# Kernel optimization log

Hardware: AMD Instinct MI355X
Metric: run time of the kernel (lower is better)

## Reference

```python
import jax, jax.numpy as jnp
import numpy as np

NEG = -10000.0

def setup_inputs() -> dict:
    key = jax.random.key(0)
    ks = jax.random.split(key, 8)
    B, S, D = 16, 1024, 768
    scale = 1.0 / np.sqrt(D)
    return {
        "q": jax.random.normal(ks[0], (B, S, D), jnp.float32),
        "k": jax.random.normal(ks[1], (B, S, D), jnp.float32),
        "v": jax.random.normal(ks[2], (B, S, D), jnp.float32),
        "Wq": jax.random.normal(ks[3], (D, D), jnp.float32) * scale,
        "bq": jnp.zeros((D,), jnp.float32),
        "Wk": jax.random.normal(ks[4], (D, D), jnp.float32) * scale,
        "bk": jnp.zeros((D,), jnp.float32),
        "Wv": jax.random.normal(ks[5], (D, D), jnp.float32) * scale,
        "bv": jnp.zeros((D,), jnp.float32),
        "temperature": jnp.float32(1.0),
    }

def reference(q, k, v, Wq, bq, Wk, bk, Wv, bv, temperature):
    # Linear projections (torch Linear: x @ W.T + b; here W stored as [out,in])
    Q = jnp.einsum("bsd,ed->bse", q, Wq) + bq  # [B,S,Dq]
    K = jnp.einsum("bsd,ed->bse", k, Wk) + bk  # [B,S,Dk]
    V = jnp.einsum("bsd,ed->bse", v, Wv) + bv  # [B,S,Dv]
    scores = jnp.einsum("bqe,bke->bqk", Q, K) / temperature  # [B,S,S]
    S = scores.shape[-1]
    diag = jnp.eye(S, dtype=bool)  # diagonal self-exclusion mask
    scores = jnp.where(diag[None, :, :], NEG, scores)
    attn = jax.nn.softmax(scores, axis=-1)
    return jnp.einsum("bqk,bke->bqe", attn, V)
```

## Files before the change

kernel.cpp:

```cpp
#include <hip/hip_runtime.h>
#include <math.h>


typedef _Float16 f16x8 __attribute__((ext_vector_type(8)));
typedef _Float16 f16x4 __attribute__((ext_vector_type(4)));
typedef __attribute__((ext_vector_type(4))) float f32x4;

template<typename T>
__device__ __forceinline__ void async_copy16(T* lds, const T* g) {
    __builtin_amdgcn_global_load_lds(
        (const __attribute__((address_space(1))) unsigned int*)g,
        (__attribute__((address_space(3))) unsigned int*)lds, 16, 0, 0);
}

__device__ __forceinline__ void barrier_mem() {
    asm volatile("s_barrier" ::: "memory");
}

template<int EPI, int BIAS>
__global__ __launch_bounds__(512, 2)
void mfma_gemm256(const _Float16* __restrict__ A, const _Float16* __restrict__ B,
                  const float* __restrict__ bias, void* __restrict__ C0,
                  int K, int lda, int ldb, int ldc,
                  long long sA, long long sB, long long sC)
{
    __shared__ _Float16 smem[65536];

    const int tid = threadIdx.x;

    const int gx = gridDim.x, gy = gridDim.y;
    const int nwg = gx * gy * gridDim.z;
    const int p = blockIdx.x + gx * (blockIdx.y + gy * blockIdx.z);
    const int cpx = nwg >> 3;
    const int l = (nwg & 7) ? p : (p & 7) * cpx + (p >> 3);
    const int bx = l % gx;
    const int by = (l / gx) % gy;
    const long long bz = l / (gx * gy);
    const int m0 = by * 256, n0 = bx * 256;

    const _Float16* A0 = A + bz * sA;
    const _Float16* B0 = B + bz * sB;

    const int lane = tid & 63;
    const int wid  = tid >> 6;
    const int wm   = wid >> 2;
    const int wn   = wid & 3;
    const int fr   = lane & 15;
    const int fs   = lane >> 4;

    const int nt = K / 64;
    const int iters = nt / 2;

    auto stage_unit = [&](int dbuf, int isB, int unit, int tile) {
        if (tile >= nt) return;
        const int kt = tile * 64;
        const int lr = tid >> 3, s = tid & 7;
        const int grow = isB ? (unit * 64 + lr)
                             : (((lr >> 5) << 7) + unit * 32 + (lr & 31));
        const int gslot = s ^ (grow & 7);
        _Float16* dst = smem + dbuf * 32768 + isB * 16384 + grow * 64 + s * 8;
        const _Float16* src = (isB ? B0 : A0)
            + (size_t)((isB ? n0 : m0) + grow) * (size_t)(isB ? ldb : lda)
            + kt + gslot * 8;
        async_copy16(dst, src);
    };

    f32x4 acc[8][4] = {};
    f16x8 bf[4][2];

#define PHASE(BUF, Q, READB, STAGES, VMW) do {                                 \
    const _Float16* Ab = smem + (BUF) * 32768;                                 \
    const _Float16* Bb = Ab + 16384;                                           \
    f16x8 a0k0, a0k1, a1k0, a1k1;                                              \
    { const int r = wm * 128 + ((Q) * 2 + 0) * 16 + fr;                        \
      a0k0 = *(const f16x8*)&Ab[r * 64 + ((fs       ^ (r & 7)) * 8)];          \
      a0k1 = *(const f16x8*)&Ab[r * 64 + (((4 + fs) ^ (r & 7)) * 8)]; }        \
    { const int r = wm * 128 + ((Q) * 2 + 1) * 16 + fr;                        \
      a1k0 = *(const f16x8*)&Ab[r * 64 + ((fs       ^ (r & 7)) * 8)];          \
      a1k1 = *(const f16x8*)&Ab[r * 64 + (((4 + fs) ^ (r & 7)) * 8)]; }        \
    if (READB) {                                                               \
      _Pragma("unroll") for (int ni = 0; ni < 4; ++ni) {                       \
        const int r = wn * 64 + ni * 16 + fr;                                  \
        bf[ni][0] = *(const f16x8*)&Bb[r * 64 + ((fs       ^ (r & 7)) * 8)];   \
        bf[ni][1] = *(const f16x8*)&Bb[r * 64 + (((4 + fs) ^ (r & 7)) * 8)]; } \
    }                                                                          \
    STAGES;                                                                    \
    barrier_mem();                                                             \
    __builtin_amdgcn_s_setprio(1);                                             \
    _Pragma("unroll") for (int ni = 0; ni < 4; ++ni) {                         \
      acc[(Q)*2+0][ni] = __builtin_amdgcn_mfma_f32_16x16x32_f16(a0k0, bf[ni][0], acc[(Q)*2+0][ni], 0, 0, 0); \
      acc[(Q)*2+0][ni] = __builtin_amdgcn_mfma_f32_16x16x32_f16(a0k1, bf[ni][1], acc[(Q)*2+0][ni], 0, 0, 0); \
      acc[(Q)*2+1][ni] = __builtin_amdgcn_mfma_f32_16x16x32_f16(a1k0, bf[ni][0], acc[(Q)*2+1][ni], 0, 0, 0); \
      acc[(Q)*2+1][ni] = __builtin_amdgcn_mfma_f32_16x16x32_f16(a1k1, bf[ni][1], acc[(Q)*2+1][ni], 0, 0, 0); \
    }                                                                          \
    __builtin_amdgcn_s_setprio(0);                                             \
    VMW;                                                                       \
    barrier_mem();                                                             \
} while (0)

    stage_unit(0, 0, 0, 0); stage_unit(0, 0, 1, 0);
    stage_unit(0, 0, 2, 0); stage_unit(0, 0, 3, 0);
    stage_unit(0, 1, 0, 0); stage_unit(0, 1, 1, 0);
    stage_unit(0, 1, 2, 0); stage_unit(0, 1, 3, 0);
    stage_unit(1, 1, 0, 1); stage_unit(1, 1, 1, 1);
    stage_unit(1, 1, 2, 1); stage_unit(1, 1, 3, 1);
    stage_unit(1, 0, 0, 1); stage_unit(1, 0, 1, 1);
    asm volatile("s_waitcnt vmcnt(6)" ::: "memory");
    barrier_mem();

    for (int i = 0; i < iters; ++i) {
        const int T1 = 2 * i + 1, T2 = 2 * i + 2, T3 = 2 * i + 3;
        const bool last = (i + 1 == iters);
        PHASE(0, 0, 1, stage_unit(1, 0, 2, T1); stage_unit(1, 0, 3, T1), );
        PHASE(0, 1, 0, stage_unit(0, 1, 0, T2); stage_unit(0, 1, 1, T2), );
        PHASE(0, 2, 0, stage_unit(0, 1, 2, T2); stage_unit(0, 1, 3, T2), );
        PHASE(0, 3, 0, stage_unit(0, 0, 0, T2); stage_unit(0, 0, 1, T2),
              if (last) { asm volatile("s_waitcnt vmcnt(0)" ::: "memory"); }
              else      { asm volatile("s_waitcnt vmcnt(6)" ::: "memory"); });
        PHASE(1, 0, 1, stage_unit(0, 0, 2, T2); stage_unit(0, 0, 3, T2), );
        PHASE(1, 1, 0, stage_unit(1, 1, 0, T3); stage_unit(1, 1, 1, T3), );
        PHASE(1, 2, 0, stage_unit(1, 1, 2, T3); stage_unit(1, 1, 3, T3), );
        PHASE(1, 3, 0, stage_unit(1, 0, 0, T3); stage_unit(1, 0, 1, T3),
              asm volatile("s_waitcnt vmcnt(6)" ::: "memory"));
    }
#undef PHASE

    #pragma unroll
    for (int mi = 0; mi < 8; ++mi) {
        #pragma unroll
        for (int ni = 0; ni < 4; ++ni) {
            const int col = n0 + wn * 64 + ni * 16 + fr;
            #pragma unroll
            for (int r = 0; r < 4; ++r) {
                const int row = m0 + wm * 128 + mi * 16 + fs * 4 + r;
                float vv = acc[mi][ni][r];
                if (BIAS == 1) vv += bias[col];
                if (BIAS == 2) vv += bias[row];
                const size_t idx = (size_t)bz * sC + (size_t)row * ldc + col;
                if (EPI == 0) ((float*)C0)[idx] = vv;
                else          ((_Float16*)C0)[idx] = (_Float16)vv;
            }
        }
    }
}

template<int EPI, int BIAS>
__global__ __launch_bounds__(256, 2)
void mfma_gemm(const _Float16* __restrict__ A, const _Float16* __restrict__ B,
               const float* __restrict__ bias,
               void* __restrict__ C0,
               int K, int lda, int ldb, int ldc,
               long long sA, long long sB, long long sC)
{
    __shared__ _Float16 sAh[128 * 32];
    __shared__ _Float16 sBh[128 * 32];

    const int tid = threadIdx.x;
    const int gx = gridDim.x, gy = gridDim.y;
    const int nwg = gx * gy * gridDim.z;
    const int p = blockIdx.x + gx * (blockIdx.y + gy * blockIdx.z);
    const int cpx = nwg >> 3;
    const int l = (nwg & 7) ? p : (p & 7) * cpx + (p >> 3);
    const int bx = l % gx;
    const int by = (l / gx) % gy;
    const long long bz = l / (gx * gy);

    const int m0 = by * 128;
    const int n0 = bx * 128;

    const _Float16* A0 = A + bz * sA;
    const _Float16* B0 = B + bz * sB;

    const int lrow  = tid >> 2;
    const int lslot = tid & 3;

    const int lane = tid & 63;
    const int wv   = tid >> 6;
    const int wm   = wv >> 1, wn = wv & 1;
    const int fr   = lane & 15;
    const int fs   = lane >> 4;
    const int sw   = fs ^ (fr & 3);
    const int abase = (wm * 64 + fr) * 32 + sw * 8;
    const int bbase = (wn * 64 + fr) * 32 + sw * 8;

    f32x4 acc[4][4] = {};

    for (int kt = 0; kt < K; kt += 32) {
        #pragma unroll
        for (int it = 0; it < 2; ++it) {
            const int row = lrow + it * 64;
            const int gsl = (lslot ^ (row & 3)) << 3;
            const size_t loff = (size_t)tid * 8 + (size_t)it * 2048;
            async_copy16(&sAh[loff], A0 + (size_t)(m0 + row) * lda + kt + gsl);
            async_copy16(&sBh[loff], B0 + (size_t)(n0 + row) * ldb + kt + gsl);
        }
        __syncthreads();

        f16x8 ah[4], bh[4];
        #pragma unroll
        for (int i = 0; i < 4; ++i) {
            ah[i] = *(const f16x8*)&sAh[abase + i * 512];
            bh[i] = *(const f16x8*)&sBh[bbase + i * 512];
        }
        #pragma unroll
        for (int mi = 0; mi < 4; ++mi)
            #pragma unroll
            for (int ni = 0; ni < 4; ++ni)
                acc[mi][ni] = __builtin_amdgcn_mfma_f32_16x16x32_f16(
                    ah[mi], bh[ni], acc[mi][ni], 0, 0, 0);
        __syncthreads();
    }

    const int er = fs * 4;
    #pragma unroll
    for (int mi = 0; mi < 4; ++mi) {
        #pragma unroll
        for (int ni = 0; ni < 4; ++ni) {
            const int col = n0 + wn * 64 + ni * 16 + fr;
            #pragma unroll
            for (int r = 0; r < 4; ++r) {
                const int row = m0 + wm * 64 + mi * 16 + er + r;
                float vv = acc[mi][ni][r];
                if (BIAS == 1) vv += bias[col];
                if (BIAS == 2) vv += bias[row];
                const size_t idx = (size_t)bz * sC + (size_t)row * ldc + col;
                if (EPI == 0) ((float*)C0)[idx] = vv;
                else          ((_Float16*)C0)[idx] = (_Float16)vv;
            }
        }
    }
}

__global__ __launch_bounds__(256)
void weights_prep(const float* __restrict__ Wq, const float* __restrict__ Wk,
                  const float* __restrict__ Wv,
                  _Float16* __restrict__ WqT, _Float16* __restrict__ WkT,
                  _Float16* __restrict__ wvh)
{
    __shared__ float t[64][65];
    const int p = blockIdx.x;
    const int tid = threadIdx.x;

    if (p < 288) {
        const long long i = ((long long)p * 256 + tid) * 8;
        const float4 a = *(const float4*)&Wv[i];
        const float4 b = *(const float4*)&Wv[i + 4];
        f16x8 o;
        o[0] = (_Float16)a.x; o[1] = (_Float16)a.y;
        o[2] = (_Float16)a.z; o[3] = (_Float16)a.w;
        o[4] = (_Float16)b.x; o[5] = (_Float16)b.y;
        o[6] = (_Float16)b.z; o[7] = (_Float16)b.w;
        *(f16x8*)&wvh[i] = o;
        return;
    }
    const int tno = p < 432 ? p - 288 : p - 432;
    const float* src = p < 432 ? Wq : Wk;
    _Float16* dst    = p < 432 ? WqT : WkT;
    const int r0 = (tno / 12) * 64, c0 = (tno % 12) * 64;
    const int tx = tid & 63, ty = tid >> 6;
    #pragma unroll
    for (int r = 0; r < 16; ++r) {
        const int row = ty * 16 + r;
        t[row][tx] = src[(size_t)(r0 + row) * 768 + c0 + tx];
    }
    __syncthreads();
    #pragma unroll
    for (int r = 0; r < 16; ++r) {
        const int orow = ty * 16 + r;
        dst[(size_t)(c0 + orow) * 768 + r0 + tx] = (_Float16)t[tx][orow];
    }
}

__global__ __launch_bounds__(256)
void colvec_kernel(const _Float16* __restrict__ WkT, const float* __restrict__ bq,
                   float* __restrict__ colvec, int n)
{
    const int wv = threadIdx.x >> 6, lane = threadIdx.x & 63;
    const int d = blockIdx.x * 4 + wv;
    float s = 0.f;
    for (int e = lane; e < n; e += 64)
        s += (float)WkT[(size_t)d * n + e] * bq[e];
    #pragma unroll
    for (int off = 32; off; off >>= 1) s += __shfl_down(s, off, 64);
    if (lane == 0) colvec[d] = s;
}

__global__ __launch_bounds__(256)
void row_prep(const float* __restrict__ k, const float* __restrict__ q,
              const float* __restrict__ v, const float* __restrict__ colvec,
              float* __restrict__ cterm, _Float16* __restrict__ kh,
              _Float16* __restrict__ qh, _Float16* __restrict__ vh)
{
    const int p = blockIdx.x;
    const int wv = threadIdx.x >> 6, lane = threadIdx.x & 63;

    if (p < 4096) {
        const long long row = (long long)p * 4 + wv;
        const float* kp = k + row * 768;
        _Float16* op = kh + row * 768;
        float s = 0.f;
        #pragma unroll
        for (int i = 0; i < 3; ++i) {
            const float4 a = *(const float4*)&kp[lane * 4 + i * 256];
            const float4 c = *(const float4*)&colvec[lane * 4 + i * 256];
            s += a.x * c.x + a.y * c.y + a.z * c.z + a.w * c.w;
            f16x4 o;
            o[0] = (_Float16)a.x; o[1] = (_Float16)a.y;
            o[2] = (_Float16)a.z; o[3] = (_Float16)a.w;
            *(f16x4*)&op[lane * 4 + i * 256] = o;
        }
        #pragma unroll
        for (int off = 32; off; off >>= 1) s += __shfl_down(s, off, 64);
        if (lane == 0) cterm[row] = s;
        return;
    }
    const int pp = p & 4095;
    const float* src = p < 8192 ? q : v;
    _Float16* dst    = p < 8192 ? qh : vh;
    const long long row = (long long)pp * 4 + wv;
    const float* sp = src + row * 768;
    _Float16* op = dst + row * 768;
    #pragma unroll
    for (int i = 0; i < 3; ++i) {
        const float4 a = *(const float4*)&sp[lane * 4 + i * 256];
        f16x4 o;
        o[0] = (_Float16)a.x; o[1] = (_Float16)a.y;
        o[2] = (_Float16)a.z; o[3] = (_Float16)a.w;
        *(f16x4*)&op[lane * 4 + i * 256] = o;
    }
}

__global__ __launch_bounds__(256)
void softmax_diag(const float* __restrict__ P, _Float16* __restrict__ Pout,
                  const float* __restrict__ tptr,
                  const float* __restrict__ cterm, int S)
{
    const int p = blockIdx.x;
    const int row = (p & 7) * (16 * 1024 / 8) + (p >> 3);
    const int i   = row % S;
    const float* rp = P + (long long)row * S;
    const int tid = threadIdx.x;
    const float invt = 1.0f / tptr[0];

    const float4 v  = *(const float4*)&rp[tid * 4];
    const float4 ct = *(const float4*)&cterm[(long long)(row / S) * S + tid * 4];
    float vals[4] = {v.x + ct.x, v.y + ct.y, v.z + ct.z, v.w + ct.w};
    #pragma unroll
    for (int j = 0; j < 4; ++j) {
        vals[j] *= invt;
        if (tid * 4 + j == i) vals[j] = -INFINITY;
    }

    float mx = fmaxf(fmaxf(vals[0], vals[1]), fmaxf(vals[2], vals[3]));
    #pragma unroll
    for (int off = 32; off > 0; off >>= 1)
        mx = fmaxf(mx, __shfl_down(mx, off, 64));

    __shared__ float smax[4], ssum[4];
    const int wv = tid >> 6, ln = tid & 63;
    if (ln == 0) smax[wv] = mx;
    __syncthreads();
    mx = fmaxf(fmaxf(smax[0], smax[1]), fmaxf(smax[2], smax[3]));

    float e[4];
    float s = 0.f;
    #pragma unroll
    for (int j = 0; j < 4; ++j) { e[j] = expf(vals[j] - mx); s += e[j]; }
    #pragma unroll
    for (int off = 32; off > 0; off >>= 1)
        s += __shfl_down(s, off, 64);
    if (ln == 0) ssum[wv] = s;
    __syncthreads();
    s = ssum[0] + ssum[1] + ssum[2] + ssum[3];

    const float inv = 1.0f / s;
    f16x4 o;
    o[0] = (_Float16)(e[0] * inv);
    o[1] = (_Float16)(e[1] * inv);
    o[2] = (_Float16)(e[2] * inv);
    o[3] = (_Float16)(e[3] * inv);
    *(f16x4*)&Pout[(long long)row * S + tid * 4] = o;
}

extern "C" void kernel_launch(void* const* d_in, const int* in_sizes, int n_in,
                              void* d_out, int out_size, void* d_ws, size_t ws_size,
                              hipStream_t stream)
{
    const float* q    = (const float*)d_in[0];
    const float* k    = (const float*)d_in[1];
    const float* v    = (const float*)d_in[2];
    const float* Wq   = (const float*)d_in[3];
    const float* bq   = (const float*)d_in[4];
    const float* Wk   = (const float*)d_in[5];
    const float* bk   = (const float*)d_in[6];
    const float* Wv   = (const float*)d_in[7];
    const float* bv   = (const float*)d_in[8];
    const float* temp = (const float*)d_in[9];
    (void)bk;

    const int S = 1024, D = 768;

    char* ws = (char*)d_ws;
    _Float16* qh  = (_Float16*)(ws + 0);
    _Float16* kh  = (_Float16*)(ws + 25165824);
    _Float16* Pc  = (_Float16*)(ws + 0);
    _Float16* vh  = (_Float16*)(ws + 50331648);
    _Float16* VT  = (_Float16*)(ws + 75497472);
    _Float16* KG  = (_Float16*)(ws + 100663296);
    float*  scores = (float*)(ws + 125829120);
    _Float16* wvh = (_Float16*)(ws + 192937984);
    _Float16* WqT = (_Float16*)(ws + 194117632);
    _Float16* WkT = (_Float16*)(ws + 195297280);
    _Float16* G   = (_Float16*)(ws + 196476928);
    float* colvec = (float*)(ws + 197656576);
    float* cterm  = (float*)(ws + 197659648);

    dim3 blk(256);
    dim3 blk512(512);

    weights_prep<<<576, blk, 0, stream>>>(Wq, Wk, Wv, WqT, WkT, wvh);
    colvec_kernel<<<192, blk, 0, stream>>>(WkT, bq, colvec, D);
    row_prep<<<12288, blk, 0, stream>>>(k, q, v, colvec, cterm, kh, qh, vh);

    mfma_gemm<1, 0><<<dim3(6, 6, 1), blk, 0, stream>>>(
        WqT, WkT, nullptr, G,
        768, 768, 768, 768, 0, 0, 0);

    mfma_gemm256<1, 0><<<dim3(3, 64, 1), blk512, 0, stream>>>(
        kh, G, nullptr, KG,
        768, 768, 768, 768, 0, 0, 0);

    mfma_gemm256<1, 2><<<dim3(4, 3, 16), blk512, 0, stream>>>(
        wvh, vh, bv, VT,
        768, 768, 768, 1024, 0, (long long)S * D, (long long)D * S);

    mfma_gemm256<0, 0><<<dim3(4, 4, 16), blk512, 0, stream>>>(
        qh, KG, nullptr, scores,
        768, 768, 768, 1024,
        (long long)S * D, (long long)S * D, (long long)S * S);

    softmax_diag<<<16 * S, blk, 0, stream>>>(scores, Pc, temp, cterm, S);

    mfma_gemm256<0, 0><<<dim3(3, 4, 16), blk512, 0, stream>>>(
        Pc, VT, nullptr, d_out,
        1024, 1024, 1024, 768,
        (long long)S * S, (long long)D * S, (long long)S * D);
}
```

Measured before the change: 216.7 us.

## Fuse bias/temperature/diag mask into scores GEMM epilogue; one-wave-per-row softmax

After: 206.0 us. -4.9%, faster.

```diff
diff --git a/kernel.cpp b/kernel.cpp
--- a/kernel.cpp
+++ b/kernel.cpp
@@ -4,7 +4,7 @@
 
 typedef _Float16 f16x8 __attribute__((ext_vector_type(8)));
 typedef _Float16 f16x4 __attribute__((ext_vector_type(4)));
-typedef __attribute__((ext_vector_type(4))) float f32x4;
+typedef float f32x4 __attribute__((ext_vector_type(4)));
 
 template<typename T>
 __device__ __forceinline__ void async_copy16(T* lds, const T* g) {
@@ -22,7 +22,8 @@
 void mfma_gemm256(const _Float16* __restrict__ A, const _Float16* __restrict__ B,
                   const float* __restrict__ bias, void* __restrict__ C0,
                   int K, int lda, int ldb, int ldc,
-                  long long sA, long long sB, long long sC)
+                  long long sA, long long sB, long long sC,
+                  const float* __restrict__ tptr, const float* __restrict__ cterm)
 {
     __shared__ _Float16 smem[65536];
 
@@ -125,6 +126,14 @@
     }
 #undef PHASE
 
+    float invt = 0.f, ct[4];
+    if (EPI == 2) {
+        invt = 1.0f / tptr[0];
+        #pragma unroll
+        for (int ni = 0; ni < 4; ++ni)
+            ct[ni] = cterm[bz * 1024 + n0 + wn * 64 + ni * 16 + fr];
+    }
+
     #pragma unroll
     for (int mi = 0; mi < 8; ++mi) {
         #pragma unroll
@@ -137,8 +146,15 @@
                 if (BIAS == 1) vv += bias[col];
                 if (BIAS == 2) vv += bias[row];
                 const size_t idx = (size_t)bz * sC + (size_t)row * ldc + col;
-                if (EPI == 0) ((float*)C0)[idx] = vv;
-                else          ((_Float16*)C0)[idx] = (_Float16)vv;
+                if (EPI == 0) {
+                    ((float*)C0)[idx] = vv;
+                } else if (EPI == 2) {
+                    vv = (vv + ct[ni]) * invt;
+                    if (row == col) vv = -INFINITY;
+                    ((float*)C0)[idx] = vv;
+                } else {
+                    ((_Float16*)C0)[idx] = (_Float16)vv;
+                }
             }
         }
     }
@@ -301,7 +317,8 @@
         float s = 0.f;
         #pragma unroll
         for (int i = 0; i < 3; ++i) {
-            const float4 a = *(const float4*)&kp[lane * 4 + i * 256];
+            const f32x4 a = __builtin_nontemporal_load(
+                (const f32x4*)&kp[lane * 4 + i * 256]);
             const float4 c = *(const float4*)&colvec[lane * 4 + i * 256];
             s += a.x * c.x + a.y * c.y + a.z * c.z + a.w * c.w;
             f16x4 o;
@@ -322,7 +339,8 @@
     _Float16* op = dst + row * 768;
     #pragma unroll
     for (int i = 0; i < 3; ++i) {
-        const float4 a = *(const float4*)&sp[lane * 4 + i * 256];
+        const f32x4 a = __builtin_nontemporal_load(
+            (const f32x4*)&sp[lane * 4 + i * 256]);
         f16x4 o;
         o[0] = (_Float16)a.x; o[1] = (_Float16)a.y;
         o[2] = (_Float16)a.z; o[3] = (_Float16)a.w;
@@ -331,55 +349,46 @@
 }
 
 __global__ __launch_bounds__(256)
-void softmax_diag(const float* __restrict__ P, _Float16* __restrict__ Pout,
-                  const float* __restrict__ tptr,
-                  const float* __restrict__ cterm, int S)
+void softmax_rows(const float* __restrict__ P, _Float16* __restrict__ Pout)
 {
     const int p = blockIdx.x;
-    const int row = (p & 7) * (16 * 1024 / 8) + (p >> 3);
-    const int i   = row % S;
-    const float* rp = P + (long long)row * S;
-    const int tid = threadIdx.x;
-    const float invt = 1.0f / tptr[0];
-
-    const float4 v  = *(const float4*)&rp[tid * 4];
-    const float4 ct = *(const float4*)&cterm[(long long)(row / S) * S + tid * 4];
-    float vals[4] = {v.x + ct.x, v.y + ct.y, v.z + ct.z, v.w + ct.w};
-    #pragma unroll
-    for (int j = 0; j < 4; ++j) {
-        vals[j] *= invt;
-        if (tid * 4 + j == i) vals[j] = -INFINITY;
-    }
-
-    float mx = fmaxf(fmaxf(vals[0], vals[1]), fmaxf(vals[2], vals[3]));
-    #pragma unroll
-    for (int off = 32; off > 0; off >>= 1)
-        mx = fmaxf(mx, __shfl_down(mx, off, 64));
-
-    __shared__ float smax[4], ssum[4];
-    const int wv = tid >> 6, ln = tid & 63;
-    if (ln == 0) smax[wv] = mx;
-    __syncthreads();
-    mx = fmaxf(fmaxf(smax[0], smax[1]), fmaxf(smax[2], smax[3]));
-
-    float e[4];
-    float s = 0.f;
-    #pragma unroll
-    for (int j = 0; j < 4; ++j) { e[j] = expf(vals[j] - mx); s += e[j]; }
-    #pragma unroll
-    for (int off = 32; off > 0; off >>= 1)
-        s += __shfl_down(s, off, 64);
-    if (ln == 0) ssum[wv] = s;
-    __syncthreads();
-    s = ssum[0] + ssum[1] + ssum[2] + ssum[3];
+    const int wv = threadIdx.x >> 6, lane = threadIdx.x & 63;
+    const int row = (p & 7) * 2048 + (p >> 3) * 4 + wv;
+    const float* rp = P + (long long)row * 1024;
+
+    float vals[16];
+    #pragma unroll
+    for (int i = 0; i < 4; ++i) {
+        const float4 a = *(const float4*)&rp[lane * 4 + i * 256];
+        vals[i * 4 + 0] = a.x; vals[i * 4 + 1] = a.y;
+        vals[i * 4 + 2] = a.z; vals[i * 4 + 3] = a.w;
+    }
+
+    float m = vals[0];
+    #pragma unroll
+    for (int j = 1; j < 16; ++j) m = fmaxf(m, vals[j]);
+    #pragma unroll
+    for (int off = 32; off; off >>= 1)
+        m = fmaxf(m, __shfl_xor(m, off, 64));
+
+    float e[16], s = 0.f;
+    #pragma unroll
+    for (int j = 0; j < 16; ++j) { e[j] = expf(vals[j] - m); s += e[j]; }
+    #pragma unroll
+    for (int off = 32; off; off >>= 1)
+        s += __shfl_xor(s, off, 64);
 
     const float inv = 1.0f / s;
-    f16x4 o;
-    o[0] = (_Float16)(e[0] * inv);
-    o[1] = (_Float16)(e[1] * inv);
-    o[2] = (_Float16)(e[2] * inv);
-    o[3] = (_Float16)(e[3] * inv);
-    *(f16x4*)&Pout[(long long)row * S + tid * 4] = o;
+    _Float16* op = Pout + (long long)row * 1024;
+    #pragma unroll
+    for (int i = 0; i < 4; ++i) {
+        f16x4 o;
+        o[0] = (_Float16)(e[i * 4 + 0] * inv);
+        o[1] = (_Float16)(e[i * 4 + 1] * inv);
+        o[2] = (_Float16)(e[i * 4 + 2] * inv);
+        o[3] = (_Float16)(e[i * 4 + 3] * inv);
+        *(f16x4*)&op[lane * 4 + i * 256] = o;
+    }
 }
 
 extern "C" void kernel_launch(void* const* d_in, const int* in_sizes, int n_in,
@@ -428,21 +437,24 @@
 
     mfma_gemm256<1, 0><<<dim3(3, 64, 1), blk512, 0, stream>>>(
         kh, G, nullptr, KG,
-        768, 768, 768, 768, 0, 0, 0);
+        768, 768, 768, 768, 0, 0, 0, nullptr, nullptr);
 
     mfma_gemm256<1, 2><<<dim3(4, 3, 16), blk512, 0, stream>>>(
         wvh, vh, bv, VT,
-        768, 768, 768, 1024, 0, (long long)S * D, (long long)D * S);
-
-    mfma_gemm256<0, 0><<<dim3(4, 4, 16), blk512, 0, stream>>>(
+        768, 768, 768, 1024, 0, (long long)S * D, (long long)D * S,
+        nullptr, nullptr);
+
+    mfma_gemm256<2, 0><<<dim3(4, 4, 16), blk512, 0, stream>>>(
         qh, KG, nullptr, scores,
         768, 768, 768, 1024,
-        (long long)S * D, (long long)S * D, (long long)S * S);
-
-    softmax_diag<<<16 * S, blk, 0, stream>>>(scores, Pc, temp, cterm, S);
+        (long long)S * D, (long long)S * D, (long long)S * S,
+        temp, cterm);
+
+    softmax_rows<<<4096, blk, 0, stream>>>(scores, Pc);
 
     mfma_gemm256<0, 0><<<dim3(3, 4, 16), blk512, 0, stream>>>(
         Pc, VT, nullptr, d_out,
         1024, 1024, 1024, 768,
-        (long long)S * S, (long long)D * S, (long long)S * D);
-}
+        (long long)S * S, (long long)D * S, (long long)S * D,
+        nullptr, nullptr);
+}
```
